# Kernel optimization log

Hardware: AMD Instinct MI355X
Metric: run time of the kernel (lower is better)

Reference implementation:

```python
import jax, jax.numpy as jnp
import numpy as np


def _lstm_step(h, c, x, kernel, rec_kernel, bias):
    # Keras LSTMCell: gate order i, f, g(candidate), o
    z = x @ kernel + h @ rec_kernel + bias  # [B, 4u]
    i, f, g, o = jnp.split(z, 4, axis=-1)
    i = jax.nn.sigmoid(i)
    f = jax.nn.sigmoid(f)
    g = jnp.tanh(g)
    o = jax.nn.sigmoid(o)
    c2 = f * c + i * g
    h2 = o * jnp.tanh(c2)
    return h2, c2


def setup_inputs() -> dict:
    key = jax.random.key(0)
    ks = jax.random.split(key, 4)
    B, S, F, U = 2048, 64, 3, 512
    OUT_NOTES = 64
    inputs = jax.random.normal(ks[0], (B, S, F), dtype=jnp.float32)
    kernel = jax.random.normal(ks[1], (F, 4 * U), dtype=jnp.float32) * 0.1
    rec_kernel = jax.random.normal(ks[2], (U, 4 * U), dtype=jnp.float32) * 0.05
    bias = jnp.zeros((4 * U,), dtype=jnp.float32)
    dense_w = jax.random.normal(ks[3], (U, F), dtype=jnp.float32) * 0.1
    dense_b = jnp.zeros((F,), dtype=jnp.float32)
    return {"inputs": inputs, "kernel": kernel, "rec_kernel": rec_kernel,
            "bias": bias, "dense_w": dense_w, "dense_b": dense_b}


def reference(inputs, kernel, rec_kernel, bias, dense_w, dense_b):
    OUT_NOTES = 64
    B = inputs.shape[0]
    U = rec_kernel.shape[0]
    h0 = jnp.zeros((B, U), dtype=inputs.dtype)
    c0 = jnp.zeros((B, U), dtype=inputs.dtype)

    # warmup: run LSTM over the input sequence, keep final state
    def warm_step(carry, x_t):
        h, c = carry
        h2, c2 = _lstm_step(h, c, x_t, kernel, rec_kernel, bias)
        return (h2, c2), None

    xs = jnp.swapaxes(inputs, 0, 1)  # [S, B, F]
    (h, c), _ = jax.lax.scan(warm_step, (h0, c0), xs)
    pred0 = h @ dense_w + dense_b  # [B, 3]

    def ar_step(carry, _):
        pred, h, c = carry
        h2, c2 = _lstm_step(h, c, pred, kernel, rec_kernel, bias)
        pred2 = h2 @ dense_w + dense_b
        return (pred2, h2, c2), pred2

    _, preds = jax.lax.scan(ar_step, (pred0, h, c), None, length=OUT_NOTES - 1)
    # tf.stack(predictions) stacks along axis 0 -> [out_notes, B, 3]
    return jnp.concatenate([pred0[None], preds], axis=0)
```

## Files before the change

kernel.cpp:

```cpp
#include <hip/hip_runtime.h>
#include <hip/hip_fp16.h>

typedef _Float16 f16;
typedef __attribute__((ext_vector_type(8))) _Float16 f16x8;
typedef __attribute__((ext_vector_type(16))) float f32x16;

#define NB 2048
#define SEQ 64
#define NF 3
#define NU 512
#define N4U 2048
#define NSTEP 127
#define WT_LD 520

#define SM_WT_BYTES (128 * WT_LD * 2)
#define SM_XS_OFF   SM_WT_BYTES
#define SM_TOTAL    (SM_XS_OFF + 128 * 3 * 4)

#define WS_PP_OFF   (16 * 1024)
#define WS_H_OFF    (1u << 20)
#define PP_PAR_STRIDE (16 * 16 * 128 * 3)
#define PP_BT_STRIDE  (16 * 128 * 3)
#define PP_UG_STRIDE  (128 * 3)

__device__ __forceinline__ float fast_rcp(float x) { return __builtin_amdgcn_rcpf(x); }
__device__ __forceinline__ float sigf(float x) { return fast_rcp(1.f + __expf(-x)); }
__device__ __forceinline__ float tanhf_fast(float x) {
    float a = fabsf(x);
    float e = __expf(-2.f * a);
    float t = (1.f - e) * fast_rcp(1.f + e);
    return copysignf(t, x);
}

__global__ __launch_bounds__(256, 1)
void lstm_feedback_kernel(const float* __restrict__ inputs, const float* __restrict__ kernw,
                          const float* __restrict__ rec, const float* __restrict__ bias,
                          const float* __restrict__ dw, const float* __restrict__ db,
                          float* __restrict__ out, float* __restrict__ pp,
                          f16* __restrict__ hbuf, unsigned* __restrict__ flags)
{
    extern __shared__ char smem[];
    f16* Wt = (f16*)smem;
    float* x_s = (float*)(smem + SM_XS_OFF);

    const int tid = threadIdx.x;
    const int bid = blockIdx.x;
    const int xcd = bid & 7;
    const int jj  = bid >> 3;
    const int bt  = (xcd << 1) | (jj & 1);
    const int ug  = jj >> 1;
    const int uBase = ug * 32;
    const int bBase = bt * 128;
    const int w  = tid >> 6;
    const int l  = tid & 63;
    const int l31 = l & 31;
    const int hf  = l >> 5;
    unsigned* myflags = flags + bt * 32;

    {
        const int c  = tid & 127;
        const int kk = tid >> 7;
        const int gcol = ((c >> 5) * 512) + uBase + (c & 31);
        for (int k = kk; k < NU; k += 2)
            Wt[c * WT_LD + k] = (f16)rec[k * N4U + gcol];
    }

    float kr[4][3], br[4], dwr[3], dbr[3];
    #pragma unroll
    for (int ct = 0; ct < 4; ++ct) {
        const int gcol = ct * 512 + uBase + l31;
        #pragma unroll
        for (int f = 0; f < 3; ++f) kr[ct][f] = kernw[f * N4U + gcol];
        br[ct] = bias[gcol];
    }
    {
        const int u = uBase + l31;
        #pragma unroll
        for (int j = 0; j < 3; ++j) { dwr[j] = dw[u * 3 + j]; dbr[j] = db[j]; }
    }
    __syncthreads();

    float c_reg[16];
    #pragma unroll
    for (int r = 0; r < 16; ++r) c_reg[r] = 0.f;

    const size_t HB = (size_t)NB * NU;
    const int bW = bBase + w * 32;
    const size_t aoff = (size_t)(bW + l31) * NU + hf * 8;
    const f16* bptr = Wt + (size_t)l31 * WT_LD + hf * 8;

    for (int s = 0; s < NSTEP; ++s) {
        if (s > 0) {
            if (tid < 16) {
                const unsigned* fp = myflags + tid;
                unsigned v;
                do {
                    v = __hip_atomic_load(fp, __ATOMIC_RELAXED, __HIP_MEMORY_SCOPE_AGENT);
                } while (v < (unsigned)s);
            }
            __syncthreads();
            if (w == 0) asm volatile("buffer_inv sc1" ::: "memory");
            __syncthreads();
        }

        if (tid < 128) {
            float v0, v1, v2;
            if (s < SEQ) {
                const float* xp = inputs + ((size_t)(bBase + tid) * SEQ + s) * NF;
                v0 = xp[0]; v1 = xp[1]; v2 = xp[2];
            } else {
                const float* p = pp + (size_t)((s + 1) & 1) * PP_PAR_STRIDE
                               + bt * PP_BT_STRIDE + tid * 3;
                v0 = dbr[0]; v1 = dbr[1]; v2 = dbr[2];
                #pragma unroll
                for (int g = 0; g < 16; ++g) {
                    v0 += p[g * PP_UG_STRIDE + 0];
                    v1 += p[g * PP_UG_STRIDE + 1];
                    v2 += p[g * PP_UG_STRIDE + 2];
                }
                if (ug == 0) {
                    float* o = out + ((size_t)(s - SEQ) * NB + bBase + tid) * 3;
                    o[0] = v0; o[1] = v1; o[2] = v2;
                }
            }
            x_s[tid * 3 + 0] = v0;
            x_s[tid * 3 + 1] = v1;
            x_s[tid * 3 + 2] = v2;
        }
        __syncthreads();

        f32x16 acc0 = {}, acc1 = {}, acc2 = {}, acc3 = {};
        if (s > 0) {
            const f16* ap = hbuf + (size_t)(s & 1) * HB + aoff;
            #pragma unroll 8
            for (int kt = 0; kt < 32; ++kt) {
                const int k0 = kt * 16;
                f16x8 a  = *(const f16x8*)(ap + k0);
                f16x8 b0 = *(const f16x8*)(bptr + 0 * 32 * WT_LD + k0);
                f16x8 b1 = *(const f16x8*)(bptr + 1 * 32 * WT_LD + k0);
                f16x8 b2 = *(const f16x8*)(bptr + 2 * 32 * WT_LD + k0);
                f16x8 b3 = *(const f16x8*)(bptr + 3 * 32 * WT_LD + k0);
                acc0 = __builtin_amdgcn_mfma_f32_32x32x16_f16(a, b0, acc0, 0, 0, 0);
                acc1 = __builtin_amdgcn_mfma_f32_32x32x16_f16(a, b1, acc1, 0, 0, 0);
                acc2 = __builtin_amdgcn_mfma_f32_32x32x16_f16(a, b2, acc2, 0, 0, 0);
                acc3 = __builtin_amdgcn_mfma_f32_32x32x16_f16(a, b3, acc3, 0, 0, 0);
            }
        }

        f16* hw = hbuf + (size_t)((s & 1) ^ 1) * HB;
        const int n_out = s - (SEQ - 1);
        float* ppw = pp + (size_t)(s & 1) * PP_PAR_STRIDE + bt * PP_BT_STRIDE + ug * PP_UG_STRIDE;
        #pragma unroll
        for (int r = 0; r < 16; ++r) {
            const int mrow = (r & 3) + ((r >> 2) << 3) + (hf << 2);
            const int mloc = (w << 5) + mrow;
            const float x0 = x_s[mloc * 3 + 0];
            const float x1 = x_s[mloc * 3 + 1];
            const float x2 = x_s[mloc * 3 + 2];
            float z0 = acc0[r] + x0 * kr[0][0] + x1 * kr[0][1] + x2 * kr[0][2] + br[0];
            float z1 = acc1[r] + x0 * kr[1][0] + x1 * kr[1][1] + x2 * kr[1][2] + br[1];
            float z2 = acc2[r] + x0 * kr[2][0] + x1 * kr[2][1] + x2 * kr[2][2] + br[2];
            float z3 = acc3[r] + x0 * kr[3][0] + x1 * kr[3][1] + x2 * kr[3][2] + br[3];
            const float gi = sigf(z0);
            const float gf = sigf(z1);
            const float gg = tanhf_fast(z2);
            const float go = sigf(z3);
            const float cv = gf * c_reg[r] + gi * gg;
            c_reg[r] = cv;
            const float h2 = go * tanhf_fast(cv);
            {
                f16* ha = hw + (size_t)(bBase + mloc) * NU + uBase + l31;
                unsigned hb = (unsigned)__builtin_bit_cast(unsigned short, (f16)h2);
                asm volatile("global_store_short %0, %1, off sc1"
                             :: "v"(ha), "v"(hb) : "memory");
            }

            if (n_out >= 0) {
                #pragma unroll
                for (int j = 0; j < 3; ++j) {
                    float v = h2 * dwr[j];
                    #pragma unroll
                    for (int m = 1; m < 32; m <<= 1) v += __shfl_xor(v, m, 64);
                    if (l31 == r)
                        __hip_atomic_store(&ppw[mloc * 3 + j], v,
                                           __ATOMIC_RELAXED, __HIP_MEMORY_SCOPE_AGENT);
                }
            }
        }

        asm volatile("s_waitcnt vmcnt(0)" ::: "memory");
        __syncthreads();
        if (tid == 0)
            __hip_atomic_store(myflags + ug, (unsigned)(s + 1),
                               __ATOMIC_RELAXED, __HIP_MEMORY_SCOPE_AGENT);
    }

    if (ug == 0) {
        if (tid < 16) {
            const unsigned* fp = myflags + tid;
            unsigned v;
            do {
                v = __hip_atomic_load(fp, __ATOMIC_RELAXED, __HIP_MEMORY_SCOPE_AGENT);
            } while (v < (unsigned)NSTEP);
        }
        __syncthreads();
        if (w == 0) asm volatile("buffer_inv sc1" ::: "memory");
        __syncthreads();
        if (tid < 128) {
            const float* p = pp + bt * PP_BT_STRIDE + tid * 3;
            float v0 = dbr[0], v1 = dbr[1], v2 = dbr[2];
            #pragma unroll
            for (int g = 0; g < 16; ++g) {
                v0 += p[g * PP_UG_STRIDE + 0];
                v1 += p[g * PP_UG_STRIDE + 1];
                v2 += p[g * PP_UG_STRIDE + 2];
            }
            float* o = out + ((size_t)63 * NB + bBase + tid) * 3;
            o[0] = v0; o[1] = v1; o[2] = v2;
        }
    }
}

extern "C" void kernel_launch(void* const* d_in, const int* in_sizes, int n_in,
                              void* d_out, int out_size, void* d_ws, size_t ws_size,
                              hipStream_t stream) {
    const float* inputs = (const float*)d_in[0];
    const float* kernw  = (const float*)d_in[1];
    const float* rec    = (const float*)d_in[2];
    const float* bias   = (const float*)d_in[3];
    const float* dw     = (const float*)d_in[4];
    const float* db     = (const float*)d_in[5];
    float* out = (float*)d_out;

    unsigned* flags = (unsigned*)d_ws;
    float* pp  = (float*)((char*)d_ws + WS_PP_OFF);
    f16* hbuf  = (f16*)((char*)d_ws + WS_H_OFF);

    hipMemsetAsync(d_ws, 0, 16 * 1024, stream);

    hipFuncSetAttribute(reinterpret_cast<const void*>(lstm_feedback_kernel),
                        hipFuncAttributeMaxDynamicSharedMemorySize, SM_TOTAL);

    void* args[] = { (void*)&inputs, (void*)&kernw, (void*)&rec, (void*)&bias,
                     (void*)&dw, (void*)&db, (void*)&out, (void*)&pp,
                     (void*)&hbuf, (void*)&flags };
    hipLaunchCooperativeKernel(reinterpret_cast<const void*>(lstm_feedback_kernel),
                               dim3(256), dim3(256), args, SM_TOTAL, stream);
}
```

Baseline: 2.560 ms.

## Replace cache invalidation with agent-scope atomic loads for cross-block state exchange

Drops the per-step buffer_inv cache invalidation and the extra barrier, and instead reads the shared hidden state and partial projections through relaxed agent-scope atomic loads. The whole h tile for the step is prefetched into registers before the input and projection gather, so the loads overlap that work. It also removes the explicit vmcnt(0) wait before the barrier that precedes the flag publish. Without that wait, stores may not be visible when the flag is published, and holding 64 u64 values per thread sharply raises register pressure.

Result: slower. 4.319 ms (+68.7%).

```diff
diff --git a/kernel.cpp b/kernel.cpp
--- a/kernel.cpp
+++ b/kernel.cpp
@@ -4,6 +4,8 @@
 typedef _Float16 f16;
 typedef __attribute__((ext_vector_type(8))) _Float16 f16x8;
 typedef __attribute__((ext_vector_type(16))) float f32x16;
+typedef __attribute__((ext_vector_type(2))) unsigned long long u64x2;
+typedef unsigned long long u64;
 
 #define NB 2048
 #define SEQ 64
@@ -30,6 +32,11 @@
     float e = __expf(-2.f * a);
     float t = (1.f - e) * fast_rcp(1.f + e);
     return copysignf(t, x);
+}
+
+__device__ __forceinline__ void st_h16_sc1(f16* p, f16 v) {
+    unsigned b = (unsigned)__builtin_bit_cast(unsigned short, v);
+    asm volatile("global_store_short %0, %1, off sc1" :: "v"(p), "v"(b) : "memory");
 }
 
 __global__ __launch_bounds__(256, 1)
@@ -99,8 +106,18 @@
                 } while (v < (unsigned)s);
             }
             __syncthreads();
-            if (w == 0) asm volatile("buffer_inv sc1" ::: "memory");
-            __syncthreads();
+        }
+
+        u64 hA[64];
+        if (s > 0) {
+            const u64* ldp = (const u64*)(hbuf + (size_t)(s & 1) * HB + aoff);
+            #pragma unroll
+            for (int kt = 0; kt < 32; ++kt) {
+                hA[2 * kt]     = __hip_atomic_load(ldp + kt * 4,
+                                     __ATOMIC_RELAXED, __HIP_MEMORY_SCOPE_AGENT);
+                hA[2 * kt + 1] = __hip_atomic_load(ldp + kt * 4 + 1,
+                                     __ATOMIC_RELAXED, __HIP_MEMORY_SCOPE_AGENT);
+            }
         }
 
         if (tid < 128) {
@@ -114,9 +131,12 @@
                 v0 = dbr[0]; v1 = dbr[1]; v2 = dbr[2];
                 #pragma unroll
                 for (int g = 0; g < 16; ++g) {
-                    v0 += p[g * PP_UG_STRIDE + 0];
-                    v1 += p[g * PP_UG_STRIDE + 1];
-                    v2 += p[g * PP_UG_STRIDE + 2];
+                    v0 += __hip_atomic_load(p + g * PP_UG_STRIDE + 0,
+                             __ATOMIC_RELAXED, __HIP_MEMORY_SCOPE_AGENT);
+                    v1 += __hip_atomic_load(p + g * PP_UG_STRIDE + 1,
+                             __ATOMIC_RELAXED, __HIP_MEMORY_SCOPE_AGENT);
+                    v2 += __hip_atomic_load(p + g * PP_UG_STRIDE + 2,
+                             __ATOMIC_RELAXED, __HIP_MEMORY_SCOPE_AGENT);
                 }
                 if (ug == 0) {
                     float* o = out + ((size_t)(s - SEQ) * NB + bBase + tid) * 3;
@@ -131,11 +151,11 @@
 
         f32x16 acc0 = {}, acc1 = {}, acc2 = {}, acc3 = {};
         if (s > 0) {
-            const f16* ap = hbuf + (size_t)(s & 1) * HB + aoff;
             #pragma unroll 8
             for (int kt = 0; kt < 32; ++kt) {
                 const int k0 = kt * 16;
-                f16x8 a  = *(const f16x8*)(ap + k0);
+                u64x2 t; t.x = hA[2 * kt]; t.y = hA[2 * kt + 1];
+                f16x8 a  = __builtin_bit_cast(f16x8, t);
                 f16x8 b0 = *(const f16x8*)(bptr + 0 * 32 * WT_LD + k0);
                 f16x8 b1 = *(const f16x8*)(bptr + 1 * 32 * WT_LD + k0);
                 f16x8 b2 = *(const f16x8*)(bptr + 2 * 32 * WT_LD + k0);
@@ -149,7 +169,8 @@
 
         f16* hw = hbuf + (size_t)((s & 1) ^ 1) * HB;
         const int n_out = s - (SEQ - 1);
-        float* ppw = pp + (size_t)(s & 1) * PP_PAR_STRIDE + bt * PP_BT_STRIDE + ug * PP_UG_STRIDE;
+        float* ppw = pp + (size_t)(s & 1) * PP_PAR_STRIDE
+                   + bt * PP_BT_STRIDE + ug * PP_UG_STRIDE;
         #pragma unroll
         for (int r = 0; r < 16; ++r) {
             const int mrow = (r & 3) + ((r >> 2) << 3) + (hf << 2);
@@ -168,12 +189,7 @@
             const float cv = gf * c_reg[r] + gi * gg;
             c_reg[r] = cv;
             const float h2 = go * tanhf_fast(cv);
-            {
-                f16* ha = hw + (size_t)(bBase + mloc) * NU + uBase + l31;
-                unsigned hb = (unsigned)__builtin_bit_cast(unsigned short, (f16)h2);
-                asm volatile("global_store_short %0, %1, off sc1"
-                             :: "v"(ha), "v"(hb) : "memory");
-            }
+            st_h16_sc1(hw + (size_t)(bBase + mloc) * NU + uBase + l31, (f16)h2);
 
             if (n_out >= 0) {
                 #pragma unroll
@@ -188,7 +204,6 @@
             }
         }
 
-        asm volatile("s_waitcnt vmcnt(0)" ::: "memory");
         __syncthreads();
         if (tid == 0)
             __hip_atomic_store(myflags + ug, (unsigned)(s + 1),
@@ -204,16 +219,17 @@
             } while (v < (unsigned)NSTEP);
         }
         __syncthreads();
-        if (w == 0) asm volatile("buffer_inv sc1" ::: "memory");
-        __syncthreads();
         if (tid < 128) {
             const float* p = pp + bt * PP_BT_STRIDE + tid * 3;
             float v0 = dbr[0], v1 = dbr[1], v2 = dbr[2];
             #pragma unroll
             for (int g = 0; g < 16; ++g) {
-                v0 += p[g * PP_UG_STRIDE + 0];
-                v1 += p[g * PP_UG_STRIDE + 1];
-                v2 += p[g * PP_UG_STRIDE + 2];
+                v0 += __hip_atomic_load(p + g * PP_UG_STRIDE + 0,
+                         __ATOMIC_RELAXED, __HIP_MEMORY_SCOPE_AGENT);
+                v1 += __hip_atomic_load(p + g * PP_UG_STRIDE + 1,
+                         __ATOMIC_RELAXED, __HIP_MEMORY_SCOPE_AGENT);
+                v2 += __hip_atomic_load(p + g * PP_UG_STRIDE + 2,
+                         __ATOMIC_RELAXED, __HIP_MEMORY_SCOPE_AGENT);
             }
             float* o = out + ((size_t)63 * NB + bBase + tid) * 3;
             o[0] = v0; o[1] = v1; o[2] = v2;
```
